# Kernel tuning notes

Measured on AMD Instinct MI355X. Metric: run time of the kernel, lower is better.

Reference implementation:

```python
import jax, jax.numpy as jnp
import numpy as np

B, CIN, H, W = 128, 3, 32, 32
C1, C2 = 64, 256
NUM_CLASSES = 1000
FC_IN = C2 * (H // 2) * (W // 2)  # 65536 after 2x2 max pool


def _n_keep(n_units, bl, Bg, n_min):
    n_local = max(1, int(n_units * bl))
    return min(n_units, max(n_min, int(n_local * (1.0 - Bg))))

K_CONV = _n_keep(C2, 0.2, 0.05, 24)      # 48
K_FC = _n_keep(FC_IN, 0.2, 0.05, 8192)   # 12451


def _conv2d(x, w, b):
    y = jax.lax.conv_general_dilated(
        x, w, window_strides=(1, 1), padding=((1, 1), (1, 1)),
        dimension_numbers=('NCHW', 'OIHW', 'NCHW'))
    return y + b[None, :, None, None]


def _maxpool2(x):
    return jax.lax.reduce_window(x, -jnp.inf, jax.lax.max,
                                 (1, 1, 2, 2), (1, 1, 2, 2), 'VALID')


def setup_inputs() -> dict:
    key = jax.random.key(0)
    ks = jax.random.split(key, 8)
    x0 = jax.random.normal(ks[0], (B, CIN, H, W), jnp.float32)
    w1 = jax.random.normal(ks[1], (C1, CIN, 3, 3), jnp.float32) * (1.0 / np.sqrt(CIN * 9))
    b1 = jax.random.normal(ks[2], (C1,), jnp.float32) * 0.01
    w2 = jax.random.normal(ks[3], (C2, C1, 3, 3), jnp.float32) * (1.0 / np.sqrt(C1 * 9))
    b2 = jax.random.normal(ks[4], (C2,), jnp.float32) * 0.01
    fc_w = jax.random.normal(ks[5], (NUM_CLASSES, FC_IN), jnp.float32) * (1.0 / np.sqrt(FC_IN))
    fc_b = jax.random.normal(ks[6], (NUM_CLASSES,), jnp.float32) * 0.01
    # gate_conv2 init: identity blocks stacked along out_channels (as in __init__)
    Wg = np.zeros((C2, C1), np.float32)
    I = np.eye(C1, dtype=np.float32)
    rows = min(C2, C1)
    Wg[:rows, :] = I[:rows, :]
    if C2 > rows:
        rep = min(C2 - rows, C1)
        Wg[rows:rows + rep, :] = I[:rep, :]
    gate_w = jnp.asarray(Wg)
    return {'x0': x0, 'w1': w1, 'b1': b1, 'gate_w': gate_w,
            'w2': w2, 'b2': b2, 'fc_w': fc_w, 'fc_b': fc_b}


def reference(x0, w1, b1, gate_w, w2, b2, fc_w, fc_b):
    # conv1 + relu
    x1 = jax.nn.relu(_conv2d(x0, w1, b1))                        # [B,C1,H,W]
    # per-out-channel scores: |x1| mean -> linear gate -> softplus (memory empty -> factor 1.0)
    sig = jnp.mean(jnp.abs(x1), axis=(0, 2, 3))                  # [C1]
    scores_c = jax.nn.softplus(gate_w @ sig)                     # [C2]
    idx_c = jax.lax.top_k(scores_c, K_CONV)[1]                   # [K_CONV]
    # conv2 on channel subset, scatter back into zeros, relu (relu commutes with zero-scatter)
    y_sel = jax.nn.relu(_conv2d(x1, w2[idx_c], b2[idx_c]))       # [B,K_CONV,H,W]
    x2 = jnp.zeros((B, C2, H, W), x0.dtype).at[:, idx_c].set(y_sel)
    # pool + flatten (C,H,W order matches torch .view)
    x_flat = _maxpool2(x2).reshape(B, -1)                        # [B,FC_IN]
    # per-feature scores and top-k feature subset
    scores_f = jnp.mean(jnp.abs(x_flat), axis=0)                 # [FC_IN]
    idx_f = jax.lax.top_k(scores_f, K_FC)[1]                     # [K_FC]
    out = x_flat[:, idx_f] @ fc_w[:, idx_f].T + fc_b             # [B,NUM_CLASSES]
    return out
```

## Files before the change

kernel.cpp:

```cpp
#include <hip/hip_runtime.h>
#include <hip/hip_bf16.h>


#define NSEL 48
#define NCLS 1000

__device__ __forceinline__ unsigned short f2bf(float x) {
  unsigned u = __builtin_bit_cast(unsigned, x);
  u += 0x7fffu + ((u >> 16) & 1u);
  return (unsigned short)(u >> 16);
}

__device__ __forceinline__ void gl_lds16(const void* g, void* l) {
  __builtin_amdgcn_global_load_lds(
      (const __attribute__((address_space(1))) void*)g,
      (__attribute__((address_space(3))) void*)l, 16, 0, 0);
}

using sh8 = __attribute__((ext_vector_type(8))) short;
using f4  = __attribute__((ext_vector_type(4))) float;

__global__ __launch_bounds__(256) void k1_conv1(
    const float* __restrict__ x0, const float* __restrict__ w1,
    const float* __restrict__ b1, unsigned short* __restrict__ x1,
    float* __restrict__ part2) {
  const int b = blockIdx.x, quarter = blockIdx.y;
  const int t = threadIdx.x;
  const int w = t >> 6, l = t & 63;
  const int ln15 = l & 15, oct = l >> 4;
  const int r0 = quarter * 8;

  __shared__ __align__(16) char smem[36864];
  __shared__ float wred[64 * 4];
  float* xs = (float*)(smem + 20480);
  short* w1t = (short*)(smem + 24320);

  for (int q = 0; q < 4; ++q) {
    const int id = q * 256 + t;
    if (id < 960) {
      const int ic = id / 320;
      const int rem = id - ic * 320;
      const int row = rem >> 5, col = rem & 31;
      const int gr = r0 - 1 + row;
      xs[id] = ((unsigned)gr < 32u)
                   ? x0[((size_t)b * 3 + ic) * 1024 + gr * 32 + col] : 0.f;
    }
  }
#pragma unroll
  for (int j = 0; j < 8; ++j) {
    const int e = j * 256 + t;
    const int oc = e & 63, k = e >> 6;
    const float v = (k < 27) ? w1[oc * 27 + k] : 0.f;
    w1t[((k >> 3) * 64 + oc) * 8 + (k & 7)] = f2bf(v);
  }
  float bias[4];
#pragma unroll
  for (int nt = 0; nt < 4; ++nt) bias[nt] = b1[nt * 16 + ln15];
  __syncthreads();

  {
    const int lr = t >> 5, pc = t & 31;
    int* prow = (int*)(smem + t * 80);
    unsigned pk2[16];
#pragma unroll
    for (int k = 0; k < 32; k += 2) {
      float v[2];
#pragma unroll
      for (int d = 0; d < 2; ++d) {
        const int kk = k + d;
        if (kk < 27) {
          const int ic = kk / 9, r9 = kk - ic * 9;
          const int kr = r9 / 3, kc = r9 - kr * 3;
          const int cc = pc + kc - 1;
          v[d] = ((unsigned)cc < 32u) ? xs[ic * 320 + (lr + kr) * 32 + cc] : 0.f;
        } else v[d] = 0.f;
      }
      pk2[k >> 1] = f2bf(v[0]) | ((unsigned)f2bf(v[1]) << 16);
    }
#pragma unroll
    for (int k2 = 0; k2 < 16; ++k2) prow[k2] = pk2[k2];
  }
  __syncthreads();

  sh8 afr[4], bfr[4];
#pragma unroll
  for (int i = 0; i < 4; ++i)
    afr[i] = *reinterpret_cast<const sh8*>(
        smem + (w * 64 + i * 16 + ln15) * 80 + oct * 16);
#pragma unroll
  for (int nt = 0; nt < 4; ++nt)
    bfr[nt] = *reinterpret_cast<const sh8*>(
        smem + 24320 + (oct * 64 + nt * 16 + ln15) * 16);
  __syncthreads();

  f4 acc[4][4];
#pragma unroll
  for (int i = 0; i < 4; ++i)
#pragma unroll
    for (int nt = 0; nt < 4; ++nt) {
      const float bv = bias[nt];
      acc[i][nt] = f4{bv, bv, bv, bv};
    }
#pragma unroll
  for (int i = 0; i < 4; ++i)
#pragma unroll
    for (int nt = 0; nt < 4; ++nt)
      acc[i][nt] = __builtin_amdgcn_mfma_f32_16x16x32_bf16(
          afr[i], bfr[nt], acc[i][nt], 0, 0, 0);

  short* po = (short*)smem;
  float wsum[4] = {0.f, 0.f, 0.f, 0.f};
#pragma unroll
  for (int i = 0; i < 4; ++i)
#pragma unroll
    for (int nt = 0; nt < 4; ++nt) {
      const f4 v = acc[i][nt];
#pragma unroll
      for (int r = 0; r < 4; ++r) {
        float x = v[r] > 0.f ? v[r] : 0.f;
        wsum[nt] += x;
        po[(w * 64 + i * 16 + oct * 4 + r) * 72 + nt * 16 + ln15] = f2bf(x);
      }
    }
#pragma unroll
  for (int nt = 0; nt < 4; ++nt) {
    float s = wsum[nt];
    s += __shfl_xor(s, 16);
    s += __shfl_xor(s, 32);
    if (l < 16) wred[(nt * 16 + ln15) * 4 + w] = s;
  }
  __syncthreads();

  {
    const int4* src = reinterpret_cast<const int4*>(smem + t * 144);
    int4* dst = reinterpret_cast<int4*>(x1) +
                ((size_t)b * 1024 + quarter * 256 + t) * 8;
#pragma unroll
    for (int j = 0; j < 8; ++j) dst[j] = src[j];
  }
  if (t < 64) {
    const float s = wred[t * 4] + wred[t * 4 + 1] + wred[t * 4 + 2] + wred[t * 4 + 3];
    part2[((size_t)quarter * 64 + t) * 128 + b] = s;
  }
}

__global__ __launch_bounds__(256) void k2_selprep(
    const float* __restrict__ part2, const float* __restrict__ gate_w,
    const float* __restrict__ w2, const float* __restrict__ b2,
    int* __restrict__ sel, unsigned short* __restrict__ w2t,
    float* __restrict__ b2s) {
  const int t = threadIdx.x;
  const int j = blockIdx.x;
  __shared__ float red[64 * 33];
  __shared__ float sig[64];
  __shared__ float sc[256];
  __shared__ int pick;

  float prt[8];
#pragma unroll
  for (int k = 0; k < 8; ++k) prt[k] = 0.f;
  const float4* pv = reinterpret_cast<const float4*>(part2);
#pragma unroll
  for (int q = 0; q < 32; ++q) {
    const float4 v = pv[q * 256 + t];
    prt[q & 7] += v.x + v.y + v.z + v.w;
  }
#pragma unroll
  for (int k = 0; k < 8; ++k)
    red[(k * 8 + (t >> 5)) * 33 + (t & 31)] = prt[k];
  __syncthreads();
  if (t < 64) {
    float s = 0.f;
    for (int i = 0; i < 32; ++i) s += red[t * 33 + i];
    sig[t] = s * (1.0f / 131072.0f);
  }
  __syncthreads();

  {
    float lg = 0.f;
#pragma unroll 8
    for (int i = 0; i < 64; ++i) lg += gate_w[t * 64 + i] * sig[i];
    sc[t] = lg;
  }
  __syncthreads();

  {
    const float v = sc[t];
    int r = 0;
    for (int i = 0; i < 256; ++i) {
      const float vi = sc[i];
      r += (vi > v) || (vi == v && i < t);
    }
    if (r == j) pick = t;
    if (j == 0 && r < NSEL) sel[r] = t;
  }
  __syncthreads();

  const int c = pick;
  if (t == 0) b2s[j] = b2[c];
  for (int id = t; id < 576; id += 256) {
    const float v = w2[(size_t)c * 576 + id];
    const int ic = id / 9;
    const int s = id - ic * 9;
    w2t[((size_t)s * 48 + j) * 64 + ic] = f2bf(v);
  }
}

__global__ __launch_bounds__(256) void k3_conv2(
    const unsigned short* __restrict__ x1, const unsigned short* __restrict__ w2t,
    const float* __restrict__ b2s, unsigned short* __restrict__ pooledt) {
  const int b = blockIdx.x, quarter = blockIdx.y;
  const int t = threadIdx.x;
  const int w = t >> 6, l = t & 63;
  const int q4 = l >> 4, ln15 = l & 15;
  __shared__ short xt[20480];

  const int r0 = quarter * 8;

  for (int q = 0; q < 10; ++q) {
    const int S = (w * 10 + q) * 64 + l;
    const int pix = S >> 3, slot = S & 7;
    const int row = pix >> 5, col = pix & 31;
    int gr = r0 - 1 + row;
    gr = gr < 0 ? 0 : (gr > 31 ? 31 : gr);
    const unsigned short* gsrc =
        x1 + ((size_t)(b * 1024 + gr * 32 + col) * 64) + (slot ^ (pix & 7)) * 8;
    gl_lds16((const void*)gsrc, (void*)&xt[(w * 10 + q) * 512]);
  }
  __syncthreads();

  f4 acc[4][3];
  const f4 fz = {0.f, 0.f, 0.f, 0.f};
#pragma unroll
  for (int i = 0; i < 4; ++i)
#pragma unroll
    for (int nt = 0; nt < 3; ++nt) acc[i][nt] = fz;

  const int w4 = w * 4;
  const sh8 zz = {0, 0, 0, 0, 0, 0, 0, 0};

#pragma unroll
  for (int kh = 0; kh < 3; ++kh)
#pragma unroll
    for (int kw = 0; kw < 3; ++kw) {
      const int sh = kh * 3 + kw;
      sh8 bf[3][2];
#pragma unroll
      for (int nt = 0; nt < 3; ++nt)
#pragma unroll
        for (int ks = 0; ks < 2; ++ks)
          bf[nt][ks] = *reinterpret_cast<const sh8*>(
              w2t + ((size_t)(sh * 48 + nt * 16 + ln15) * 64 + ks * 32 + q4 * 8));
#pragma unroll
      for (int i = 0; i < 4; ++i) {
        const int mt = w4 + i;
        const int lsr = (mt >> 1) + kh;
        const int gsr = r0 + lsr - 1;
        if ((unsigned)gsr < 32u) {
          const int w_ = (mt & 1) * 16 + ln15;
          const int cc = w_ + kw - 1;
          const bool cv = (unsigned)cc < 32u;
          int p = lsr * 32 + cc;
          p = p < 0 ? 0 : (p > 319 ? 319 : p);
#pragma unroll
          for (int ks = 0; ks < 2; ++ks) {
            sh8 af = *reinterpret_cast<const sh8*>(
                &xt[p * 64 + (((ks << 2) | q4) ^ (p & 7)) * 8]);
            af = cv ? af : zz;
            acc[i][0] = __builtin_amdgcn_mfma_f32_16x16x32_bf16(af, bf[0][ks], acc[i][0], 0, 0, 0);
            acc[i][1] = __builtin_amdgcn_mfma_f32_16x16x32_bf16(af, bf[1][ks], acc[i][1], 0, 0, 0);
            acc[i][2] = __builtin_amdgcn_mfma_f32_16x16x32_bf16(af, bf[2][ks], acc[i][2], 0, 0, 0);
          }
        }
      }
    }

  __syncthreads();

  float bias[3];
#pragma unroll
  for (int nt = 0; nt < 3; ++nt) bias[nt] = b2s[nt * 16 + ln15];

  unsigned short* ps = reinterpret_cast<unsigned short*>(xt);
#pragma unroll
  for (int a = 0; a < 2; ++a) {
#pragma unroll
    for (int nt = 0; nt < 3; ++nt) {
      const f4 A = acc[a][nt], Bv = acc[a + 2][nt];
#pragma unroll
      for (int pr = 0; pr < 2; ++pr) {
        float m = fmaxf(fmaxf(A[pr * 2], A[pr * 2 + 1]),
                        fmaxf(Bv[pr * 2], Bv[pr * 2 + 1]));
        m = fmaxf(m + bias[nt], 0.f);
        const int pl = w * 16 + a * 8 + q4 * 2 + pr;
        ps[(nt * 16 + ln15) * 64 + pl] = f2bf(m);
      }
    }
  }
  __syncthreads();

  const int4* psv = reinterpret_cast<const int4*>(xt);
  int4* po = reinterpret_cast<int4*>(pooledt);
  for (int c = t; c < 384; c += 256) {
    const int j = c >> 3, sub = c & 7;
    po[(size_t)(j * 32 + quarter * 8 + sub) * 128 + b] = psv[c];
  }
}

__global__ __launch_bounds__(256) void k4_fc(
    const unsigned short* __restrict__ pooledt, const float* __restrict__ fc_w,
    const int* __restrict__ sel, float* __restrict__ fcpart) {
  const int ntile = blockIdx.x;
  const int ks = blockIdx.y;
  const int t = threadIdx.x;
  const int w = t >> 6, l = t & 63;

  __shared__ short Ab[2][8192];
  __shared__ short Bb[2][2048];

  f4 acc[2][2];
  const f4 fzero = {0.f, 0.f, 0.f, 0.f};
#pragma unroll
  for (int i = 0; i < 2; ++i)
#pragma unroll
    for (int j = 0; j < 2; ++j) acc[i][j] = fzero;

  int chs[6];
#pragma unroll
  for (int i = 0; i < 6; ++i)
    chs[i] = __builtin_amdgcn_readfirstlane(sel[(ks * 6 + i) >> 2]);

  const int n0 = ntile * 32;
  const int nl = t & 31;
  int ng = n0 + nl; if (ng > 999) ng = 999;
  const int kh = t >> 5;
  const float* wrow = fc_w + (size_t)ng * 65536 + kh * 8;

  const int4* pt = reinterpret_cast<const int4*>(pooledt);
  const int kb0 = ks * 48;

  int4 av[4];
  float4 bv0, bv1;

  {
#pragma unroll
    for (int it = 0; it < 4; ++it) {
      const int s = it * 256 + t, ko = s >> 7, m = s & 127;
      av[it] = pt[(kb0 + ko) * 128 + m];
    }
    const float* bp = wrow + chs[0] * 256 + ((ks * 6) & 3) * 64;
    bv0 = *reinterpret_cast<const float4*>(bp);
    bv1 = *reinterpret_cast<const float4*>(bp + 4);
#pragma unroll
    for (int it = 0; it < 4; ++it)
      *reinterpret_cast<int4*>(&Ab[0][(it * 256 + t) * 8]) = av[it];
    int4 bw;
    bw.x = f2bf(bv0.x) | ((unsigned)f2bf(bv0.y) << 16);
    bw.y = f2bf(bv0.z) | ((unsigned)f2bf(bv0.w) << 16);
    bw.z = f2bf(bv1.x) | ((unsigned)f2bf(bv1.y) << 16);
    bw.w = f2bf(bv1.z) | ((unsigned)f2bf(bv1.w) << 16);
    *reinterpret_cast<int4*>(&Bb[0][(kh * 32 + nl) * 8]) = bw;
  }
  __syncthreads();

  for (int tt = 0; tt < 6; ++tt) {
    const int cur = tt & 1, nxt = cur ^ 1;
    if (tt < 5) {
      const int tn = tt + 1;
#pragma unroll
      for (int it = 0; it < 4; ++it) {
        const int s = it * 256 + t, ko = s >> 7, m = s & 127;
        av[it] = pt[(kb0 + tn * 8 + ko) * 128 + m];
      }
      const float* bp = wrow + chs[tn] * 256 + ((ks * 6 + tn) & 3) * 64;
      bv0 = *reinterpret_cast<const float4*>(bp);
      bv1 = *reinterpret_cast<const float4*>(bp + 4);
    }

#pragma unroll
    for (int s2 = 0; s2 < 2; ++s2) {
      const int kg = s2 * 4 + (l >> 4);
      const int m0 = w * 32 + (l & 15);
      sh8 a0 = *reinterpret_cast<const sh8*>(&Ab[cur][(kg * 128 + m0) * 8]);
      sh8 a1 = *reinterpret_cast<const sh8*>(&Ab[cur][(kg * 128 + m0 + 16) * 8]);
      sh8 b0 = *reinterpret_cast<const sh8*>(&Bb[cur][(kg * 32 + (l & 15)) * 8]);
      sh8 b1 = *reinterpret_cast<const sh8*>(&Bb[cur][(kg * 32 + 16 + (l & 15)) * 8]);
      acc[0][0] = __builtin_amdgcn_mfma_f32_16x16x32_bf16(a0, b0, acc[0][0], 0, 0, 0);
      acc[0][1] = __builtin_amdgcn_mfma_f32_16x16x32_bf16(a0, b1, acc[0][1], 0, 0, 0);
      acc[1][0] = __builtin_amdgcn_mfma_f32_16x16x32_bf16(a1, b0, acc[1][0], 0, 0, 0);
      acc[1][1] = __builtin_amdgcn_mfma_f32_16x16x32_bf16(a1, b1, acc[1][1], 0, 0, 0);
    }

    if (tt < 5) {
#pragma unroll
      for (int it = 0; it < 4; ++it)
        *reinterpret_cast<int4*>(&Ab[nxt][(it * 256 + t) * 8]) = av[it];
      int4 bw;
      bw.x = f2bf(bv0.x) | ((unsigned)f2bf(bv0.y) << 16);
      bw.y = f2bf(bv0.z) | ((unsigned)f2bf(bv0.w) << 16);
      bw.z = f2bf(bv1.x) | ((unsigned)f2bf(bv1.y) << 16);
      bw.w = f2bf(bv1.z) | ((unsigned)f2bf(bv1.w) << 16);
      *reinterpret_cast<int4*>(&Bb[nxt][(kh * 32 + nl) * 8]) = bw;
    }
    __syncthreads();
  }

  const int r0 = (l >> 4) * 4;
#pragma unroll
  for (int fm = 0; fm < 2; ++fm)
#pragma unroll
    for (int fn = 0; fn < 2; ++fn)
#pragma unroll
      for (int r = 0; r < 4; ++r) {
        const int m = w * 32 + fm * 16 + r0 + r;
        const int nc = n0 + fn * 16 + (l & 15);
        fcpart[(((size_t)ks * 128 + m) << 10) + nc] = acc[fm][fn][r];
      }
}

__global__ __launch_bounds__(256) void k5_reduce(
    const float* __restrict__ fcpart, const float* __restrict__ fc_b,
    float* __restrict__ out) {
  const int id = blockIdx.x * 256 + threadIdx.x;
  const int b = id / 1000;
  const int n = id - b * 1000;
  float s = fc_b[n];
#pragma unroll
  for (int ks = 0; ks < 32; ++ks)
    s += fcpart[(((size_t)ks * 128 + b) << 10) + n];
  out[id] = s;
}

extern "C" void kernel_launch(void* const* d_in, const int* in_sizes, int n_in,
                              void* d_out, int out_size, void* d_ws, size_t ws_size,
                              hipStream_t stream) {
  (void)in_sizes; (void)n_in; (void)out_size; (void)ws_size;
  const float* x0     = (const float*)d_in[0];
  const float* w1     = (const float*)d_in[1];
  const float* b1     = (const float*)d_in[2];
  const float* gate_w = (const float*)d_in[3];
  const float* w2     = (const float*)d_in[4];
  const float* b2     = (const float*)d_in[5];
  const float* fc_w   = (const float*)d_in[6];
  const float* fc_b   = (const float*)d_in[7];
  float* out = (float*)d_out;

  char* ws = (char*)d_ws;
  unsigned short* x1      = (unsigned short*)(ws);
  unsigned short* pooledt = (unsigned short*)(ws + 16777216);
  float*          part2   = (float*)(ws + 19922944);
  int*            sel     = (int*)  (ws + 20054016);
  unsigned short* w2t     = (unsigned short*)(ws + 20054272);
  float*          b2s     = (float*)(ws + 20109568);
  float*          fcpart  = (float*)(ws + 20110336);

  hipLaunchKernelGGL(k1_conv1, dim3(128, 4), dim3(256), 0, stream, x0, w1, b1, x1, part2);
  hipLaunchKernelGGL(k2_selprep, dim3(48), dim3(256), 0, stream, part2, gate_w, w2, b2, sel, w2t, b2s);
  hipLaunchKernelGGL(k3_conv2, dim3(128, 4), dim3(256), 0, stream, x1, w2t, b2s, pooledt);
  hipLaunchKernelGGL(k4_fc, dim3(32, 32), dim3(256), 0, stream, pooledt, fc_w, sel, fcpart);
  hipLaunchKernelGGL(k5_reduce, dim3(500), dim3(256), 0, stream, fcpart, fc_b, out);
}
```

Measured before the change: 70.84 us.

## Stage gate weights in LDS, coalesce FC weight loads, store FC partials as bf16

k2 now copies gate_w into padded shared memory before the gate matvec, so each thread no longer reads its own strided row from global memory. k4 remaps the fc_w loads so eight adjacent lanes read contiguous 64-float spans of one output row, and pads the B tile in LDS (stride 33) to avoid bank conflicts. The split-K partial sums are written and read as bf16 instead of fp32, halving that intermediate traffic. Rounding the partials to bf16 before the 32-way reduction adds numerical error.

Result: no change. 69.66 us (median of 2 runs) (-1.7%).

```diff
diff --git a/kernel.cpp b/kernel.cpp
--- a/kernel.cpp
+++ b/kernel.cpp
@@ -9,6 +9,10 @@
   unsigned u = __builtin_bit_cast(unsigned, x);
   u += 0x7fffu + ((u >> 16) & 1u);
   return (unsigned short)(u >> 16);
+}
+
+__device__ __forceinline__ float bf2f(unsigned short u) {
+  return __builtin_bit_cast(float, (unsigned)u << 16);
 }
 
 __device__ __forceinline__ void gl_lds16(const void* g, void* l) {
@@ -151,11 +155,23 @@
     float* __restrict__ b2s) {
   const int t = threadIdx.x;
   const int j = blockIdx.x;
+  __shared__ float gw[256 * 65];
   __shared__ float red[64 * 33];
   __shared__ float sig[64];
   __shared__ float sc[256];
   __shared__ int pick;
 
+  {
+    const float4* gv = reinterpret_cast<const float4*>(gate_w);
+#pragma unroll
+    for (int i = 0; i < 16; ++i) {
+      const int f = i * 256 + t;
+      const float4 v = gv[f];
+      float* d = &gw[(f >> 4) * 65 + (f & 15) * 4];
+      d[0] = v.x; d[1] = v.y; d[2] = v.z; d[3] = v.w;
+    }
+  }
+
   float prt[8];
 #pragma unroll
   for (int k = 0; k < 8; ++k) prt[k] = 0.f;
@@ -179,7 +195,7 @@
   {
     float lg = 0.f;
 #pragma unroll 8
-    for (int i = 0; i < 64; ++i) lg += gate_w[t * 64 + i] * sig[i];
+    for (int i = 0; i < 64; ++i) lg += gw[t * 65 + i] * sig[i];
     sc[t] = lg;
   }
   __syncthreads();
@@ -309,21 +325,17 @@
 
 __global__ __launch_bounds__(256) void k4_fc(
     const unsigned short* __restrict__ pooledt, const float* __restrict__ fc_w,
-    const int* __restrict__ sel, float* __restrict__ fcpart) {
+    const int* __restrict__ sel, unsigned short* __restrict__ fcpart) {
   const int ntile = blockIdx.x;
   const int ks = blockIdx.y;
   const int t = threadIdx.x;
   const int w = t >> 6, l = t & 63;
+  const int ln15 = l & 15;
 
   __shared__ short Ab[2][8192];
-  __shared__ short Bb[2][2048];
-
-  f4 acc[2][2];
-  const f4 fzero = {0.f, 0.f, 0.f, 0.f};
-#pragma unroll
-  for (int i = 0; i < 2; ++i)
-#pragma unroll
-    for (int j = 0; j < 2; ++j) acc[i][j] = fzero;
+  __shared__ short Bb[2][8 * 33 * 8];
+
+  f4 acc00 = {0.f, 0.f, 0.f, 0.f}, acc01 = acc00, acc10 = acc00, acc11 = acc00;
 
   int chs[6];
 #pragma unroll
@@ -331,10 +343,9 @@
     chs[i] = __builtin_amdgcn_readfirstlane(sel[(ks * 6 + i) >> 2]);
 
   const int n0 = ntile * 32;
-  const int nl = t & 31;
-  int ng = n0 + nl; if (ng > 999) ng = 999;
-  const int kh = t >> 5;
-  const float* wrow = fc_w + (size_t)ng * 65536 + kh * 8;
+  const int bn = w * 8 + (l >> 3);
+  int ngb = n0 + bn; if (ngb > 999) ngb = 999;
+  const float* brow = fc_w + (size_t)ngb * 65536 + (l & 7) * 8;
 
   const int4* pt = reinterpret_cast<const int4*>(pooledt);
   const int kb0 = ks * 48;
@@ -342,84 +353,73 @@
   int4 av[4];
   float4 bv0, bv1;
 
-  {
-#pragma unroll
-    for (int it = 0; it < 4; ++it) {
-      const int s = it * 256 + t, ko = s >> 7, m = s & 127;
-      av[it] = pt[(kb0 + ko) * 128 + m];
-    }
-    const float* bp = wrow + chs[0] * 256 + ((ks * 6) & 3) * 64;
-    bv0 = *reinterpret_cast<const float4*>(bp);
-    bv1 = *reinterpret_cast<const float4*>(bp + 4);
-#pragma unroll
-    for (int it = 0; it < 4; ++it)
-      *reinterpret_cast<int4*>(&Ab[0][(it * 256 + t) * 8]) = av[it];
-    int4 bw;
-    bw.x = f2bf(bv0.x) | ((unsigned)f2bf(bv0.y) << 16);
-    bw.y = f2bf(bv0.z) | ((unsigned)f2bf(bv0.w) << 16);
-    bw.z = f2bf(bv1.x) | ((unsigned)f2bf(bv1.y) << 16);
-    bw.w = f2bf(bv1.z) | ((unsigned)f2bf(bv1.w) << 16);
-    *reinterpret_cast<int4*>(&Bb[0][(kh * 32 + nl) * 8]) = bw;
-  }
+#define LOADAB(tn)                                                        \
+  {                                                                       \
+    _Pragma("unroll") for (int it = 0; it < 4; ++it) {                    \
+      const int s = it * 256 + t;                                         \
+      av[it] = pt[(kb0 + (tn) * 8 + (s >> 7)) * 128 + (s & 127)];         \
+    }                                                                     \
+    const float* bp = brow + chs[tn] * 256 + ((ks * 6 + (tn)) & 3) * 64;  \
+    bv0 = *reinterpret_cast<const float4*>(bp);                           \
+    bv1 = *reinterpret_cast<const float4*>(bp + 4);                       \
+  }
+#define WRITEAB(buf)                                                      \
+  {                                                                       \
+    _Pragma("unroll") for (int it = 0; it < 4; ++it)                      \
+      *reinterpret_cast<int4*>(&Ab[buf][(it * 256 + t) * 8]) = av[it];    \
+    int4 bw;                                                              \
+    bw.x = f2bf(bv0.x) | ((unsigned)f2bf(bv0.y) << 16);                   \
+    bw.y = f2bf(bv0.z) | ((unsigned)f2bf(bv0.w) << 16);                   \
+    bw.z = f2bf(bv1.x) | ((unsigned)f2bf(bv1.y) << 16);                   \
+    bw.w = f2bf(bv1.z) | ((unsigned)f2bf(bv1.w) << 16);                   \
+    *reinterpret_cast<int4*>(&Bb[buf][((l & 7) * 33 + bn) * 8]) = bw;     \
+  }
+
+  LOADAB(0);
+  WRITEAB(0);
   __syncthreads();
 
   for (int tt = 0; tt < 6; ++tt) {
     const int cur = tt & 1, nxt = cur ^ 1;
-    if (tt < 5) {
-      const int tn = tt + 1;
-#pragma unroll
-      for (int it = 0; it < 4; ++it) {
-        const int s = it * 256 + t, ko = s >> 7, m = s & 127;
-        av[it] = pt[(kb0 + tn * 8 + ko) * 128 + m];
-      }
-      const float* bp = wrow + chs[tn] * 256 + ((ks * 6 + tn) & 3) * 64;
-      bv0 = *reinterpret_cast<const float4*>(bp);
-      bv1 = *reinterpret_cast<const float4*>(bp + 4);
-    }
+    if (tt < 5) LOADAB(tt + 1);
 
 #pragma unroll
     for (int s2 = 0; s2 < 2; ++s2) {
       const int kg = s2 * 4 + (l >> 4);
-      const int m0 = w * 32 + (l & 15);
+      const int m0 = w * 32 + ln15;
       sh8 a0 = *reinterpret_cast<const sh8*>(&Ab[cur][(kg * 128 + m0) * 8]);
       sh8 a1 = *reinterpret_cast<const sh8*>(&Ab[cur][(kg * 128 + m0 + 16) * 8]);
-      sh8 b0 = *reinterpret_cast<const sh8*>(&Bb[cur][(kg * 32 + (l & 15)) * 8]);
-      sh8 b1 = *reinterpret_cast<const sh8*>(&Bb[cur][(kg * 32 + 16 + (l & 15)) * 8]);
-      acc[0][0] = __builtin_amdgcn_mfma_f32_16x16x32_bf16(a0, b0, acc[0][0], 0, 0, 0);
-      acc[0][1] = __builtin_amdgcn_mfma_f32_16x16x32_bf16(a0, b1, acc[0][1], 0, 0, 0);
-      acc[1][0] = __builtin_amdgcn_mfma_f32_16x16x32_bf16(a1, b0, acc[1][0], 0, 0, 0);
-      acc[1][1] = __builtin_amdgcn_mfma_f32_16x16x32_bf16(a1, b1, acc[1][1], 0, 0, 0);
-    }
-
-    if (tt < 5) {
-#pragma unroll
-      for (int it = 0; it < 4; ++it)
-        *reinterpret_cast<int4*>(&Ab[nxt][(it * 256 + t) * 8]) = av[it];
-      int4 bw;
-      bw.x = f2bf(bv0.x) | ((unsigned)f2bf(bv0.y) << 16);
-      bw.y = f2bf(bv0.z) | ((unsigned)f2bf(bv0.w) << 16);
-      bw.z = f2bf(bv1.x) | ((unsigned)f2bf(bv1.y) << 16);
-      bw.w = f2bf(bv1.z) | ((unsigned)f2bf(bv1.w) << 16);
-      *reinterpret_cast<int4*>(&Bb[nxt][(kh * 32 + nl) * 8]) = bw;
-    }
+      sh8 b0 = *reinterpret_cast<const sh8*>(&Bb[cur][(kg * 33 + ln15) * 8]);
+      sh8 b1 = *reinterpret_cast<const sh8*>(&Bb[cur][(kg * 33 + 16 + ln15) * 8]);
+      acc00 = __builtin_amdgcn_mfma_f32_16x16x32_bf16(a0, b0, acc00, 0, 0, 0);
+      acc01 = __builtin_amdgcn_mfma_f32_16x16x32_bf16(a0, b1, acc01, 0, 0, 0);
+      acc10 = __builtin_amdgcn_mfma_f32_16x16x32_bf16(a1, b0, acc10, 0, 0, 0);
+      acc11 = __builtin_amdgcn_mfma_f32_16x16x32_bf16(a1, b1, acc11, 0, 0, 0);
+    }
+
+    if (tt < 5) WRITEAB(nxt);
     __syncthreads();
   }
+#undef LOADAB
+#undef WRITEAB
 
   const int r0 = (l >> 4) * 4;
 #pragma unroll
   for (int fm = 0; fm < 2; ++fm)
 #pragma unroll
-    for (int fn = 0; fn < 2; ++fn)
+    for (int fn = 0; fn < 2; ++fn) {
+      const f4 a = fm == 0 ? (fn == 0 ? acc00 : acc01) : (fn == 0 ? acc10 : acc11);
 #pragma unroll
       for (int r = 0; r < 4; ++r) {
         const int m = w * 32 + fm * 16 + r0 + r;
-        const int nc = n0 + fn * 16 + (l & 15);
-        fcpart[(((size_t)ks * 128 + m) << 10) + nc] = acc[fm][fn][r];
+        const int nc = n0 + fn * 16 + ln15;
+        fcpart[(((size_t)ks * 128 + m) << 10) + nc] = f2bf(a[r]);
       }
+    }
 }
 
 __global__ __launch_bounds__(256) void k5_reduce(
-    const float* __restrict__ fcpart, const float* __restrict__ fc_b,
+    const unsigned short* __restrict__ fcpart, const float* __restrict__ fc_b,
     float* __restrict__ out) {
   const int id = blockIdx.x * 256 + threadIdx.x;
   const int b = id / 1000;
@@ -427,7 +427,7 @@
   float s = fc_b[n];
 #pragma unroll
   for (int ks = 0; ks < 32; ++ks)
-    s += fcpart[(((size_t)ks * 128 + b) << 10) + n];
+    s += bf2f(fcpart[(((size_t)ks * 128 + b) << 10) + n]);
   out[id] = s;
 }
 
@@ -452,7 +452,7 @@
   int*            sel     = (int*)  (ws + 20054016);
   unsigned short* w2t     = (unsigned short*)(ws + 20054272);
   float*          b2s     = (float*)(ws + 20109568);
-  float*          fcpart  = (float*)(ws + 20110336);
+  unsigned short* fcpart  = (unsigned short*)(ws + 20110336);
 
   hipLaunchKernelGGL(k1_conv1, dim3(128, 4), dim3(256), 0, stream, x0, w1, b1, x1, part2);
   hipLaunchKernelGGL(k2_selprep, dim3(48), dim3(256), 0, stream, part2, gate_w, w2, b2, sel, w2t, b2s);
```
